# Optimization experiments

Measured on AMD Instinct MI355X. Metric: run time of the kernel, lower is better.

## Reference

```python
import jax, jax.numpy as jnp
import numpy as np

HIDDEN = 1024
HEADS = 16
HEAD_DIM = HIDDEN // HEADS
SCALE = HEAD_DIM ** -0.5
NEG_INF = -1e9  # finite stand-in for -inf so silu(masked) -> ~0 instead of NaN


def setup_inputs() -> dict:
    key = jax.random.key(0)
    ks = jax.random.split(key, 12)
    B, Sq, Sk = 2, 2048, 2048
    inp = {
        "query": jax.random.normal(ks[0], (B, Sq, HIDDEN), jnp.float32),
        "key": jax.random.normal(ks[1], (B, Sk, HIDDEN), jnp.float32),
        "value": jax.random.normal(ks[2], (B, Sk, HIDDEN), jnp.float32),
        "mask": jax.random.randint(ks[3], (B, 1, Sq, Sk), 0, 2, jnp.int32),
        # torch nn.Linear weights are [out_features, in_features]
        "Wq": jax.random.normal(ks[4], (HIDDEN, HIDDEN), jnp.float32) * 0.02,
        "bq": jax.random.normal(ks[5], (HIDDEN,), jnp.float32) * 0.02,
        "Wk": jax.random.normal(ks[6], (HIDDEN, HIDDEN), jnp.float32) * 0.02,
        "bk": jax.random.normal(ks[7], (HIDDEN,), jnp.float32) * 0.02,
        "Wv": jax.random.normal(ks[8], (HIDDEN, HIDDEN), jnp.float32) * 0.02,
        "bv": jax.random.normal(ks[9], (HIDDEN,), jnp.float32) * 0.02,
        "Wo": jax.random.normal(ks[10], (HIDDEN, HIDDEN), jnp.float32) * 0.02,
    }
    return inp


def _split_heads(x):
    B, S, _ = x.shape
    return x.reshape(B, S, HEADS, HEAD_DIM).transpose(0, 2, 1, 3)  # [B,H,S,D]


def reference(query, key, value, mask, Wq, bq, Wk, bk, Wv, bv, Wo):
    B, Sq, _ = query.shape
    q = _split_heads(query @ Wq.T + bq)   # [B,H,Sq,D]
    k = _split_heads(key @ Wk.T + bk)     # [B,H,Sk,D]
    v = _split_heads(value @ Wv.T + bv)   # [B,H,Sk,D]
    scores = jnp.einsum("bhqd,bhkd->bhqk", q, k) * SCALE
    scores = jnp.where(mask == 0, NEG_INF, scores)
    attn = jax.nn.silu(scores)            # silu in place of softmax (per source)
    # dropout is identity in eval mode
    out = jnp.einsum("bhqk,bhkd->bhqd", attn, v)
    out = out.transpose(0, 2, 1, 3).reshape(B, Sq, HIDDEN)
    return out @ Wo.T  # o_proj has no bias
```

## Files before the change

kernel.cpp:

```cpp
#include <hip/hip_runtime.h>
#include <hip/hip_bf16.h>

typedef __attribute__((ext_vector_type(4))) float f32x4;
typedef __attribute__((ext_vector_type(16))) float f32x16;
typedef __attribute__((ext_vector_type(8))) short short8;
typedef __attribute__((ext_vector_type(4))) unsigned int uint4v;

__device__ __forceinline__ unsigned short f2bf(float f) {
  unsigned int u = __float_as_uint(f);
  u += 0x7fffu + ((u >> 16) & 1u);
  return (unsigned short)(u >> 16);
}

__device__ __forceinline__ void g2lds16(const void* g, void* l) {
  __builtin_amdgcn_global_load_lds(
      (const __attribute__((address_space(1))) void*)g,
      (__attribute__((address_space(3))) void*)l, 16, 0, 0);
}

__global__ __launch_bounds__(256) void prep(
    const float* __restrict__ q, const float* __restrict__ k,
    const float* __restrict__ v, const float* __restrict__ Wq,
    const float* __restrict__ Wk, const float* __restrict__ Wv,
    const float* __restrict__ Wo, const int* __restrict__ mask,
    unsigned short* __restrict__ xq, unsigned short* __restrict__ xk,
    unsigned short* __restrict__ xv, unsigned short* __restrict__ wqb,
    unsigned short* __restrict__ wkb, unsigned short* __restrict__ wvb,
    unsigned short* __restrict__ wob, unsigned int* __restrict__ mbT) {
  const int y = blockIdx.y;
  const int idx = blockIdx.x * 256 + (int)threadIdx.x;
  if (y == 4) {
#pragma unroll
    for (int it = 0; it < 8; ++it) {
      const int i = blockIdx.x * 2048 + it * 256 + (int)threadIdx.x;
      const unsigned long long bits = __ballot(mask[i] != 0);
      if ((threadIdx.x & 63) == 0) {
        const int row = i >> 11;
        const int j = (i & 2047) >> 5;
        mbT[j * 4096 + row] = (unsigned int)bits;
        mbT[(j + 1) * 4096 + row] = (unsigned int)(bits >> 32);
      }
    }
    return;
  }
  const float* s;
  unsigned short* d;
  int i = idx;
  if (y == 0)      { s = q; d = xq; }
  else if (y == 1) { s = k; d = xk; }
  else if (y == 2) { s = v; d = xv; }
  else {
    const int wsel = idx >> 18;
    i = idx & 0x3FFFF;
    s = wsel == 0 ? Wq : (wsel == 1 ? Wk : (wsel == 2 ? Wv : Wo));
    d = wsel == 0 ? wqb : (wsel == 1 ? wkb : (wsel == 2 ? wvb : wob));
  }
  const float4 val = ((const float4*)s)[i];
  ushort4 o;
  o.x = f2bf(val.x); o.y = f2bf(val.y); o.z = f2bf(val.z); o.w = f2bf(val.w);
  ((ushort4*)d)[i] = o;
}

__global__ __launch_bounds__(256) void add_bf16(const unsigned short* __restrict__ a,
                                                const unsigned short* __restrict__ b,
                                                unsigned short* __restrict__ o) {
  const int i = blockIdx.x * 256 + threadIdx.x;
  const short8 va = ((const short8*)a)[i];
  const short8 vb = ((const short8*)b)[i];
  short8 vo;
#pragma unroll
  for (int j = 0; j < 8; ++j) {
    const float fa = __uint_as_float((unsigned int)(unsigned short)va[j] << 16);
    const float fb = __uint_as_float((unsigned int)(unsigned short)vb[j] << 16);
    vo[j] = (short)f2bf(fa + fb);
  }
  ((short8*)o)[i] = vo;
}

template <int BIAS_MODE, int OUT_BF16>
__device__ __forceinline__ void gemm_tile(
    unsigned short* __restrict__ As, unsigned short* __restrict__ Bs,
    const unsigned short* __restrict__ A, const unsigned short* __restrict__ B,
    const float* __restrict__ bias, void* __restrict__ Cp,
    const int N, const int K, const int m0, const int n0, const float cscale) {
  const int tid  = (int)threadIdx.x;
  const int lane = tid & 63;
  const int wm   = tid >> 7;
  const int wn   = (tid >> 6) & 1;

  const f32x4 vzero = {0.f, 0.f, 0.f, 0.f};
  f32x4 acc[4][4];
#pragma unroll
  for (int mr = 0; mr < 4; ++mr)
#pragma unroll
    for (int nr = 0; nr < 4; ++nr) acc[mr][nr] = vzero;

  for (int k0 = 0; k0 < K; k0 += 64) {
#pragma unroll
    for (int i = 0; i < 4; ++i) {
      const int idx = i * 256 + tid;
      const int r = idx >> 3;
      const int c = idx & 7;
      const int koff = k0 + ((c ^ (r & 7)) << 3);
      g2lds16(A + (size_t)(m0 + r) * K + koff, &As[(i * 256 + (tid & 192)) * 8]);
      g2lds16(B + (size_t)(n0 + r) * K + koff, &Bs[(i * 256 + (tid & 192)) * 8]);
    }
    __syncthreads();
#pragma unroll
    for (int kk = 0; kk < 2; ++kk) {
      short8 af[4], bf[4];
#pragma unroll
      for (int mr = 0; mr < 4; ++mr) {
        const int row = wm * 64 + mr * 16 + (lane & 15);
        const int ch = (kk * 4 + (lane >> 4)) ^ (row & 7);
        af[mr] = *(const short8*)&As[row * 64 + ch * 8];
      }
#pragma unroll
      for (int nr = 0; nr < 4; ++nr) {
        const int row = wn * 64 + nr * 16 + (lane & 15);
        const int ch = (kk * 4 + (lane >> 4)) ^ (row & 7);
        bf[nr] = *(const short8*)&Bs[row * 64 + ch * 8];
      }
#pragma unroll
      for (int mr = 0; mr < 4; ++mr)
#pragma unroll
        for (int nr = 0; nr < 4; ++nr)
          acc[mr][nr] = __builtin_amdgcn_mfma_f32_16x16x32_bf16(af[mr], bf[nr],
                                                                acc[mr][nr], 0, 0, 0);
    }
    __syncthreads();
  }

#pragma unroll
  for (int mr = 0; mr < 4; ++mr) {
#pragma unroll
    for (int nr = 0; nr < 4; ++nr) {
#pragma unroll
      for (int rg = 0; rg < 4; ++rg) {
        const int row = m0 + wm * 64 + mr * 16 + ((lane >> 4) << 2) + rg;
        const int col = n0 + wn * 64 + nr * 16 + (lane & 15);
        float v = acc[mr][nr][rg];
        if (BIAS_MODE == 1) v += bias[col];
        if (BIAS_MODE == 2) v += bias[row];
        v *= cscale;
        if (OUT_BF16) ((unsigned short*)Cp)[(size_t)row * N + col] = f2bf(v);
        else          ((float*)Cp)[(size_t)row * N + col] = v;
      }
    }
  }
}

#define QSCALE 0.18033688011112042f
#define LN2    0.6931471805599453f

__global__ __launch_bounds__(256) void proj_qkv(
    const unsigned short* __restrict__ xq, const unsigned short* __restrict__ xk,
    const unsigned short* __restrict__ xv,
    const unsigned short* __restrict__ wq, const unsigned short* __restrict__ wk,
    const unsigned short* __restrict__ wv,
    const float* __restrict__ bq, const float* __restrict__ bk,
    const float* __restrict__ bv,
    unsigned short* __restrict__ qp, unsigned short* __restrict__ kp,
    unsigned short* __restrict__ vt) {
  __shared__ unsigned short As[128 * 64];
  __shared__ unsigned short Bs[128 * 64];
  const int z = blockIdx.z;
  if (z == 0) {
    gemm_tile<1, 1>(As, Bs, xq, wq, bq, qp, 1024, 1024, blockIdx.y * 128, blockIdx.x * 128, QSCALE);
  } else if (z == 1) {
    gemm_tile<1, 1>(As, Bs, xk, wk, bk, kp, 1024, 1024, blockIdx.y * 128, blockIdx.x * 128, 1.0f);
  } else {
    gemm_tile<2, 1>(As, Bs, wv, xv, bv, vt, 4096, 1024, blockIdx.x * 128, blockIdx.y * 128, 1.0f);
  }
}

__global__ __launch_bounds__(512) void out_proj8(
    const unsigned short* __restrict__ ao, const unsigned short* __restrict__ wo,
    float* __restrict__ out) {
  __shared__ unsigned short SM[4][128 * 64];

  const int tid  = (int)threadIdx.x;
  const int lane = tid & 63;
  const int wm = tid >> 8;
  const int wn = (tid >> 7) & 1;
  const int kh = (tid >> 6) & 1;
  const int m0 = blockIdx.y * 128;
  const int n0 = blockIdx.x * 128;

  const f32x4 vzero = {0.f, 0.f, 0.f, 0.f};
  f32x4 acc[4][4];
#pragma unroll
  for (int mr = 0; mr < 4; ++mr)
#pragma unroll
    for (int nr = 0; nr < 4; ++nr) acc[mr][nr] = vzero;

  for (int j = 0; j < 8; ++j) {
#pragma unroll
    for (int i = 0; i < 2; ++i) {
      const int idx = i * 512 + tid;
      const int r = idx >> 3;
      const int cc = idx & 7;
      const int cs = (cc ^ (r & 7)) << 3;
      const int wb = (i * 512 + (tid & 448)) * 8;
      g2lds16(ao + (size_t)(m0 + r) * 1024 + j * 64 + cs,       &SM[0][wb]);
      g2lds16(ao + (size_t)(m0 + r) * 1024 + 512 + j * 64 + cs, &SM[1][wb]);
      g2lds16(wo + (size_t)(n0 + r) * 1024 + j * 64 + cs,       &SM[2][wb]);
      g2lds16(wo + (size_t)(n0 + r) * 1024 + 512 + j * 64 + cs, &SM[3][wb]);
    }
    __syncthreads();
#pragma unroll
    for (int kk = 0; kk < 2; ++kk) {
      short8 af[4], bf[4];
#pragma unroll
      for (int mr = 0; mr < 4; ++mr) {
        const int row = wm * 64 + mr * 16 + (lane & 15);
        const int ch = (kk * 4 + (lane >> 4)) ^ (row & 7);
        af[mr] = *(const short8*)&SM[kh][row * 64 + ch * 8];
      }
#pragma unroll
      for (int nr = 0; nr < 4; ++nr) {
        const int row = wn * 64 + nr * 16 + (lane & 15);
        const int ch = (kk * 4 + (lane >> 4)) ^ (row & 7);
        bf[nr] = *(const short8*)&SM[2 + kh][row * 64 + ch * 8];
      }
#pragma unroll
      for (int mr = 0; mr < 4; ++mr)
#pragma unroll
        for (int nr = 0; nr < 4; ++nr)
          acc[mr][nr] = __builtin_amdgcn_mfma_f32_16x16x32_bf16(af[mr], bf[nr],
                                                                acc[mr][nr], 0, 0, 0);
    }
    __syncthreads();
  }

  float* red = (float*)SM;
  const int reg4 = wm * 2 + wn;
  if (kh) {
#pragma unroll
    for (int mr = 0; mr < 4; ++mr)
#pragma unroll
      for (int nr = 0; nr < 4; ++nr)
#pragma unroll
        for (int g = 0; g < 4; ++g)
          red[reg4 * 4096 + lane * 64 + ((mr * 16 + nr * 4 + g + lane) & 63)] = acc[mr][nr][g];
  }
  __syncthreads();
  if (!kh) {
#pragma unroll
    for (int mr = 0; mr < 4; ++mr)
#pragma unroll
      for (int nr = 0; nr < 4; ++nr)
#pragma unroll
        for (int g = 0; g < 4; ++g) {
          const float v = acc[mr][nr][g] +
              red[reg4 * 4096 + lane * 64 + ((mr * 16 + nr * 4 + g + lane) & 63)];
          const int row = m0 + wm * 64 + mr * 16 + ((lane >> 4) << 2) + g;
          const int col = n0 + wn * 64 + nr * 16 + (lane & 15);
          out[(size_t)row * 1024 + col] = v;
        }
  }
}

__global__ __launch_bounds__(256, 4) void attn_kernel(
    const unsigned short* __restrict__ qp, const unsigned short* __restrict__ kp,
    const unsigned short* __restrict__ vt, const unsigned int* __restrict__ mbT,
    unsigned short* __restrict__ ao0, unsigned short* __restrict__ ao1) {
  __shared__ unsigned short SMEM[2][2][64 * 64];

  const int tid  = (int)threadIdx.x;
  const int lane = tid & 63;
  const int w    = tid >> 6;
  const int qsub = w >> 1;
  const int kh   = w & 1;
  const int c32  = lane & 31;
  const int lo   = lane >> 5;
  const int qbase = blockIdx.x * 64;
  const int h  = blockIdx.y;
  const int b  = blockIdx.z >> 1;
  const int ks = blockIdx.z & 1;
  const size_t tok0 = (size_t)b * 2048;
  const int kbase = ks * 1024;

  const int q = qbase + qsub * 32 + c32;
  const unsigned short* qptr = qp + (tok0 + q) * 1024 + h * 64 + lo * 8;
  short8 qf[4];
#pragma unroll
  for (int kd = 0; kd < 4; ++kd) qf[kd] = *(const short8*)(qptr + kd * 16);

  const unsigned int* mql = mbT + (size_t)(ks * 32 + kh) * 4096 + tok0 + q;

  f32x16 oacc[2];
#pragma unroll
  for (int dt = 0; dt < 2; ++dt)
#pragma unroll
    for (int r = 0; r < 16; ++r) oacc[dt][r] = 0.f;

  auto stage = [&](int kt_, int bf_) {
#pragma unroll
    for (int i = 0; i < 2; ++i) {
      const int idx = i * 256 + tid;
      const int r = idx >> 3;
      const int cc = idx & 7;
      const int cs = (cc ^ (r & 7)) << 3;
      const int wb = (i * 256 + (tid & 192)) * 8;
      g2lds16(kp + (tok0 + kbase + kt_ * 64 + r) * 1024 + h * 64 + cs, &SMEM[bf_][0][wb]);
      g2lds16(vt + (size_t)(h * 64 + r) * 4096 + tok0 + kbase + kt_ * 64 + cs, &SMEM[bf_][1][wb]);
    }
  };

  stage(0, 0);
  __syncthreads();

  const f32x16 z16 = {0.f};
  for (int kt = 0; kt < 16; ++kt) {
    const int buf = kt & 1;
    if (kt < 15) stage(kt + 1, buf ^ 1);
    const unsigned int mcur = mql[(size_t)kt * 8192];

    f32x16 st = z16;
    __builtin_amdgcn_s_setprio(1);
#pragma unroll
    for (int kd = 0; kd < 4; ++kd) {
      const int krt = kh * 32 + c32;
      const short8 kf = *(const short8*)&SMEM[buf][0][krt * 64 + (((2 * kd + lo) ^ (c32 & 7)) << 3)];
      st = __builtin_amdgcn_mfma_f32_32x32x16_bf16(kf, qf[kd], st, 0, 0, 0);
    }
    __builtin_amdgcn_s_setprio(0);

    const unsigned int ms = mcur >> (lo * 4);
#pragma unroll
    for (int r = 0; r < 16; ++r) {
      const int krow = (r & 3) + 8 * (r >> 2);
      const int smear = __builtin_amdgcn_sbfe((int)ms, krow, 1);
      const float sv = __int_as_float(__float_as_int(st[r]) & smear);
      st[r] = sv * __builtin_amdgcn_rcpf(1.f + __builtin_amdgcn_exp2f(-sv));
    }

    unsigned int u[8];
#pragma unroll
    for (int g = 0; g < 4; ++g) {
      asm("v_cvt_pk_bf16_f32 %0, %1, %2" : "=v"(u[2 * g])     : "v"(st[4 * g]),     "v"(st[4 * g + 1]));
      asm("v_cvt_pk_bf16_f32 %0, %1, %2" : "=v"(u[2 * g + 1]) : "v"(st[4 * g + 2]), "v"(st[4 * g + 3]));
    }
    asm("v_permlane32_swap_b32 %0, %1" : "+v"(u[0]), "+v"(u[2]));
    asm("v_permlane32_swap_b32 %0, %1" : "+v"(u[1]), "+v"(u[3]));
    asm("v_permlane32_swap_b32 %0, %1" : "+v"(u[4]), "+v"(u[6]));
    asm("v_permlane32_swap_b32 %0, %1" : "+v"(u[5]), "+v"(u[7]));
    const uint4v wA = {u[0], u[1], u[2], u[3]};
    const uint4v wB = {u[4], u[5], u[6], u[7]};
    const short8 paA = __builtin_bit_cast(short8, wA);
    const short8 paB = __builtin_bit_cast(short8, wB);

    __builtin_amdgcn_s_setprio(1);
#pragma unroll
    for (int dt = 0; dt < 2; ++dt) {
      const int drow = dt * 32 + c32;
      const short8 vf0 = *(const short8*)&SMEM[buf][1][drow * 64 + (((4 * kh + lo) ^ (c32 & 7)) << 3)];
      const short8 vf1 = *(const short8*)&SMEM[buf][1][drow * 64 + (((4 * kh + 2 + lo) ^ (c32 & 7)) << 3)];
      oacc[dt] = __builtin_amdgcn_mfma_f32_32x32x16_bf16(paA, vf0, oacc[dt], 0, 0, 0);
      oacc[dt] = __builtin_amdgcn_mfma_f32_32x32x16_bf16(paB, vf1, oacc[dt], 0, 0, 0);
    }
    __builtin_amdgcn_s_setprio(0);

    __syncthreads();
  }

  float* red = (float*)SMEM;
  const int rbase = qsub * 2048;
  if (kh) {
#pragma unroll
    for (int dt = 0; dt < 2; ++dt)
#pragma unroll
      for (int r = 0; r < 16; ++r)
        red[rbase + lane * 32 + ((dt * 16 + r + lane) & 31)] = oacc[dt][r];
  }
  __syncthreads();
  if (!kh) {
    unsigned short* aop = ks ? ao1 : ao0;
#pragma unroll
    for (int dt = 0; dt < 2; ++dt)
#pragma unroll
      for (int r = 0; r < 16; ++r) {
        const float o2 = oacc[dt][r] + red[rbase + lane * 32 + ((dt * 16 + r + lane) & 31)];
        const int row = qbase + qsub * 32 + (r & 3) + 8 * (r >> 2) + 4 * lo;
        const int col = h * 64 + dt * 32 + c32;
        aop[(tok0 + row) * 1024 + col] = f2bf(o2 * LN2);
      }
  }
}

extern "C" void kernel_launch(void* const* d_in, const int* in_sizes, int n_in,
                              void* d_out, int out_size, void* d_ws, size_t ws_size,
                              hipStream_t stream) {
  (void)in_sizes; (void)n_in; (void)out_size; (void)ws_size;
  const float* query = (const float*)d_in[0];
  const float* key   = (const float*)d_in[1];
  const float* value = (const float*)d_in[2];
  const int*   mask  = (const int*)d_in[3];
  const float* Wq = (const float*)d_in[4];
  const float* bq = (const float*)d_in[5];
  const float* Wk = (const float*)d_in[6];
  const float* bk = (const float*)d_in[7];
  const float* Wv = (const float*)d_in[8];
  const float* bv = (const float*)d_in[9];
  const float* Wo = (const float*)d_in[10];

  char* ws = (char*)d_ws;
  const size_t MB = 1024 * 1024;
  unsigned short* xq  = (unsigned short*)(ws + 0 * MB);
  unsigned short* xk  = (unsigned short*)(ws + 8 * MB);
  unsigned short* xv  = (unsigned short*)(ws + 16 * MB);
  unsigned short* wqb = (unsigned short*)(ws + 24 * MB);
  unsigned short* wkb = (unsigned short*)(ws + 26 * MB);
  unsigned short* wvb = (unsigned short*)(ws + 28 * MB);
  unsigned short* wob = (unsigned short*)(ws + 30 * MB);
  unsigned short* qp  = (unsigned short*)(ws + 32 * MB);
  unsigned short* kp  = (unsigned short*)(ws + 40 * MB);
  unsigned short* vt  = (unsigned short*)(ws + 48 * MB);
  unsigned int*   mbT = (unsigned int*)(ws + 56 * MB);
  unsigned short* ao  = xq;
  unsigned short* ap0 = xk;
  unsigned short* ap1 = xv;

  prep<<<dim3(4096, 5), 256, 0, stream>>>(query, key, value, Wq, Wk, Wv, Wo, mask,
                                          xq, xk, xv, wqb, wkb, wvb, wob, mbT);

  proj_qkv<<<dim3(8, 32, 3), 256, 0, stream>>>(xq, xk, xv, wqb, wkb, wvb,
                                               bq, bk, bv, qp, kp, vt);
  attn_kernel<<<dim3(32, 16, 4), 256, 0, stream>>>(qp, kp, vt, mbT, ap0, ap1);
  add_bf16<<<2048, 256, 0, stream>>>(ap0, ap1, ao);
  out_proj8<<<dim3(8, 32), 512, 0, stream>>>(ao, wob, (float*)d_out);
}
```

Baseline: 163.0 us.

## Load K/V fragments directly from global memory in attention, remap blocks per XCD

The attention kernel stops staging K and V tiles into double-buffered shared memory and drops the per-iteration barrier. Each wave now reads its MFMA operands straight from global memory and relies on the L2/MALL caches for reuse across waves and blocks. The launch becomes a 1D grid whose index is remapped so blocks sharing a head land on the same XCD, and the occupancy hint rises from 4 to 6 now that LDS is only used for the final reduction. In exchange, every wave issues its own uncoalesced global loads, and their latency is no longer hidden by an explicit prefetch stage.

```diff
diff --git a/kernel.cpp b/kernel.cpp
--- a/kernel.cpp
+++ b/kernel.cpp
@@ -261,11 +261,11 @@
   }
 }
 
-__global__ __launch_bounds__(256, 4) void attn_kernel(
+__global__ __launch_bounds__(256, 6) void attn_kernel(
     const unsigned short* __restrict__ qp, const unsigned short* __restrict__ kp,
     const unsigned short* __restrict__ vt, const unsigned int* __restrict__ mbT,
     unsigned short* __restrict__ ao0, unsigned short* __restrict__ ao1) {
-  __shared__ unsigned short SMEM[2][2][64 * 64];
+  __shared__ float red[4096];
 
   const int tid  = (int)threadIdx.x;
   const int lane = tid & 63;
@@ -274,10 +274,17 @@
   const int kh   = w & 1;
   const int c32  = lane & 31;
   const int lo   = lane >> 5;
-  const int qbase = blockIdx.x * 64;
-  const int h  = blockIdx.y;
-  const int b  = blockIdx.z >> 1;
-  const int ks = blockIdx.z & 1;
+
+  const int flat = (int)blockIdx.x;
+  const int xcd  = flat & 7;
+  const int rest = flat >> 3;
+  const int x    = rest & 31;
+  const int cmb  = xcd + ((rest >> 5) << 3);
+  const int h  = cmb & 15;
+  const int z  = cmb >> 4;
+  const int qbase = x * 64;
+  const int b  = z >> 1;
+  const int ks = z & 1;
   const size_t tok0 = (size_t)b * 2048;
   const int kbase = ks * 1024;
 
@@ -287,7 +294,11 @@
 #pragma unroll
   for (int kd = 0; kd < 4; ++kd) qf[kd] = *(const short8*)(qptr + kd * 16);
 
-  const unsigned int* mql = mbT + (size_t)(ks * 32 + kh) * 4096 + tok0 + q;
+  const unsigned int* mp = mbT + (size_t)(ks * 32 + kh) * 4096 + tok0 + q;
+
+  const unsigned short* kgl = kp + (tok0 + kbase + kh * 32 + c32) * 1024 + h * 64 + lo * 8;
+  const unsigned short* vg0 = vt + (size_t)(h * 64 + c32) * 4096 + tok0 + kbase + lo * 8;
+  const unsigned short* vg1 = vg0 + (size_t)32 * 4096;
 
   f32x16 oacc[2];
 #pragma unroll
@@ -295,36 +306,19 @@
 #pragma unroll
     for (int r = 0; r < 16; ++r) oacc[dt][r] = 0.f;
 
-  auto stage = [&](int kt_, int bf_) {
-#pragma unroll
-    for (int i = 0; i < 2; ++i) {
-      const int idx = i * 256 + tid;
-      const int r = idx >> 3;
-      const int cc = idx & 7;
-      const int cs = (cc ^ (r & 7)) << 3;
-      const int wb = (i * 256 + (tid & 192)) * 8;
-      g2lds16(kp + (tok0 + kbase + kt_ * 64 + r) * 1024 + h * 64 + cs, &SMEM[bf_][0][wb]);
-      g2lds16(vt + (size_t)(h * 64 + r) * 4096 + tok0 + kbase + kt_ * 64 + cs, &SMEM[bf_][1][wb]);
-    }
-  };
-
-  stage(0, 0);
-  __syncthreads();
-
   const f32x16 z16 = {0.f};
+
+#pragma unroll 2
   for (int kt = 0; kt < 16; ++kt) {
-    const int buf = kt & 1;
-    if (kt < 15) stage(kt + 1, buf ^ 1);
-    const unsigned int mcur = mql[(size_t)kt * 8192];
+    const unsigned int mcur = mp[(size_t)kt * 8192];
+    const unsigned short* kb = kgl + (size_t)kt * 65536;
 
     f32x16 st = z16;
     __builtin_amdgcn_s_setprio(1);
-#pragma unroll
-    for (int kd = 0; kd < 4; ++kd) {
-      const int krt = kh * 32 + c32;
-      const short8 kf = *(const short8*)&SMEM[buf][0][krt * 64 + (((2 * kd + lo) ^ (c32 & 7)) << 3)];
-      st = __builtin_amdgcn_mfma_f32_32x32x16_bf16(kf, qf[kd], st, 0, 0, 0);
-    }
+    st = __builtin_amdgcn_mfma_f32_32x32x16_bf16(*(const short8*)(kb),      qf[0], st, 0, 0, 0);
+    st = __builtin_amdgcn_mfma_f32_32x32x16_bf16(*(const short8*)(kb + 16), qf[1], st, 0, 0, 0);
+    st = __builtin_amdgcn_mfma_f32_32x32x16_bf16(*(const short8*)(kb + 32), qf[2], st, 0, 0, 0);
+    st = __builtin_amdgcn_mfma_f32_32x32x16_bf16(*(const short8*)(kb + 48), qf[3], st, 0, 0, 0);
     __builtin_amdgcn_s_setprio(0);
 
     const unsigned int ms = mcur >> (lo * 4);
@@ -351,21 +345,15 @@
     const short8 paA = __builtin_bit_cast(short8, wA);
     const short8 paB = __builtin_bit_cast(short8, wB);
 
+    const int vo = kt * 64 + kh * 32;
     __builtin_amdgcn_s_setprio(1);
-#pragma unroll
-    for (int dt = 0; dt < 2; ++dt) {
-      const int drow = dt * 32 + c32;
-      const short8 vf0 = *(const short8*)&SMEM[buf][1][drow * 64 + (((4 * kh + lo) ^ (c32 & 7)) << 3)];
-      const short8 vf1 = *(const short8*)&SMEM[buf][1][drow * 64 + (((4 * kh + 2 + lo) ^ (c32 & 7)) << 3)];
-      oacc[dt] = __builtin_amdgcn_mfma_f32_32x32x16_bf16(paA, vf0, oacc[dt], 0, 0, 0);
-      oacc[dt] = __builtin_amdgcn_mfma_f32_32x32x16_bf16(paB, vf1, oacc[dt], 0, 0, 0);
-    }
+    oacc[0] = __builtin_amdgcn_mfma_f32_32x32x16_bf16(paA, *(const short8*)(vg0 + vo),      oacc[0], 0, 0, 0);
+    oacc[0] = __builtin_amdgcn_mfma_f32_32x32x16_bf16(paB, *(const short8*)(vg0 + vo + 16), oacc[0], 0, 0, 0);
+    oacc[1] = __builtin_amdgcn_mfma_f32_32x32x16_bf16(paA, *(const short8*)(vg1 + vo),      oacc[1], 0, 0, 0);
+    oacc[1] = __builtin_amdgcn_mfma_f32_32x32x16_bf16(paB, *(const short8*)(vg1 + vo + 16), oacc[1], 0, 0, 0);
     __builtin_amdgcn_s_setprio(0);
-
-    __syncthreads();
-  }
-
-  float* red = (float*)SMEM;
+  }
+
   const int rbase = qsub * 2048;
   if (kh) {
 #pragma unroll
@@ -427,7 +415,7 @@
 
   proj_qkv<<<dim3(8, 32, 3), 256, 0, stream>>>(xq, xk, xv, wqb, wkb, wvb,
                                                bq, bk, bv, qp, kp, vt);
-  attn_kernel<<<dim3(32, 16, 4), 256, 0, stream>>>(qp, kp, vt, mbT, ap0, ap1);
+  attn_kernel<<<dim3(2048), 256, 0, stream>>>(qp, kp, vt, mbT, ap0, ap1);
   add_bf16<<<2048, 256, 0, stream>>>(ap0, ap1, ao);
   out_proj8<<<dim3(8, 32), 512, 0, stream>>>(ao, wob, (float*)d_out);
 }
```

New measurement: 357.6 us. +119.3%, slower.
